# Kernel tuning notes

Measured on AMD Instinct MI355X. Metric: run time of the kernel, lower is better.

## Reference

```python
import jax, jax.numpy as jnp
import numpy as np

H, D = 8, 16
HD = H * D
SCALE0 = float(1.0 / np.sqrt(D * 1))   # degree-0 dot-product scale (order m=1)
SCALE1 = float(1.0 / np.sqrt(D * 3))   # degree-1 dot-product scale (order m=3)
SHARED = float(np.sqrt(0.5))           # shared_scale = sqrt(1/2) for DOT_PROD + SHARED
NEG = -1e9


def _split_heads_q(x):  # (b,n,HD,m) -> (b,H,n,D,m)
    b, n, _, m = x.shape
    return x.reshape(b, n, H, D, m).transpose(0, 2, 1, 3, 4)


def _split_heads_k(x):  # (b,n,N,HD,m) -> (b,H,n,N,D,m)
    b, n, N, _, m = x.shape
    return x.reshape(b, n, N, H, D, m).transpose(0, 3, 1, 2, 4, 5)


def _augment_kv(k, v, feats, W_self, null_k, null_v):
    # attend_self: VNLinear self key/value; use_null_kv: learned null tokens.
    b, n = feats.shape[:2]
    m = feats.shape[-1]
    skv = jnp.einsum('oc,bncm->bnom', W_self, feats)          # (b,n,2HD,m)
    sk, sv = jnp.split(skv, 2, axis=-2)
    sk = _split_heads_q(sk)[:, :, :, None]                     # (b,H,n,1,D,m)
    sv = _split_heads_q(sv)[:, :, :, None]
    nk = jnp.broadcast_to(null_k[None, :, None, None], (b, H, n, 1, D, m))
    nv = jnp.broadcast_to(null_v[None, :, None, None], (b, H, n, 1, D, m))
    k = jnp.concatenate([nk, sk, k], axis=3)                   # (b,H,n,2+N,D,m)
    v = jnp.concatenate([nv, sv, v], axis=3)
    return k, v


def _merge_heads(x):  # (b,H,n,D,m) -> (b,n,HD,m)
    b, _, n, _, m = x.shape
    return x.transpose(0, 2, 1, 3, 4).reshape(b, n, HD, m)


def _forward(q0, k0, v0, q1, k1, v1, feats0, feats1, edges,
             W_self_kv0, W_self_kv1, W_bias, self_bias, null_bias,
             null_k0, null_v0, null_k1, null_v1, head_weights1,
             W_out0, W_out1, neighbor_mask):
    b, n, N = edges.shape[:3]
    q0h, k0h, v0h = _split_heads_q(q0), _split_heads_k(k0), _split_heads_k(v0)
    q1h, k1h, v1h = _split_heads_q(q1), _split_heads_k(k1), _split_heads_k(v1)
    k0h, v0h = _augment_kv(k0h, v0h, feats0, W_self_kv0, null_k0, null_v0)
    k1h, v1h = _augment_kv(k1h, v1h, feats1, W_self_kv1, null_k1, null_v1)

    # pair bias for degree 0 (to_order==1); prepend null/self bias columns
    edge_bias = jnp.einsum('bnje,he->bhnj', edges, W_bias)     # (b,H,n,N)
    nb = jnp.broadcast_to(null_bias[None, :, None, None], (b, H, n, 1))
    sb = jnp.broadcast_to(self_bias[None, :, None, None], (b, H, n, 1))
    bias = jnp.concatenate([nb, sb, edge_bias], axis=-1)        # (b,H,n,2+N)

    sim0 = jnp.einsum('bhndm,bhnjdm->bhnj', q0h, k0h) * SCALE0 + bias
    w1 = jax.nn.softplus(head_weights1)                         # (1,H,1,1)
    sim1 = jnp.einsum('bhndm,bhnjdm->bhnj', q1h, k1h) * (SCALE1 * w1)

    total = (sim0 + sim1) * SHARED
    mask = jnp.concatenate(
        [jnp.ones((b, 1, n, 2), dtype=bool),                    # null + self always valid
         neighbor_mask[:, None]], axis=-1)
    total = jnp.where(mask, total, NEG)
    attn = jax.nn.softmax(total, axis=-1)                       # shared across degrees

    out0 = _merge_heads(jnp.einsum('bhnj,bhnjdm->bhndm', attn, v0h))
    out1 = _merge_heads(jnp.einsum('bhnj,bhnjdm->bhndm', attn, v1h))

    y0 = jnp.einsum('oc,bncm->bnom', W_out0, out0)              # FiberLinear deg 0
    y1 = jnp.einsum('oc,bncm->bnom', W_out1, out1)              # FiberLinear deg 1
    return y0, y1


def setup_inputs() -> dict:
    key = jax.random.key(0)
    ks = jax.random.split(key, 20)
    b, n, N, e = 1, 2048, 32, 32
    d0, d1 = 128, 64
    f = lambda k, s: jax.random.normal(k, s, dtype=jnp.float32) * 0.1
    return {
        'q0': f(ks[0], (b, n, HD, 1)), 'k0': f(ks[1], (b, n, N, HD, 1)), 'v0': f(ks[2], (b, n, N, HD, 1)),
        'q1': f(ks[3], (b, n, HD, 3)), 'k1': f(ks[4], (b, n, N, HD, 3)), 'v1': f(ks[5], (b, n, N, HD, 3)),
        'feats0': f(ks[6], (b, n, d0, 1)), 'feats1': f(ks[7], (b, n, d1, 3)),
        'edges': f(ks[8], (b, n, N, e)),
        'W_self_kv0': f(ks[9], (2 * HD, d0)), 'W_self_kv1': f(ks[10], (2 * HD, d1)),
        'W_bias': f(ks[11], (H, e)),
        'self_bias': jnp.zeros((H,), jnp.float32), 'null_bias': jnp.zeros((H,), jnp.float32),
        'null_k0': jnp.zeros((H, D, 1), jnp.float32), 'null_v0': jnp.zeros((H, D, 1), jnp.float32),
        'null_k1': jnp.zeros((H, D, 3), jnp.float32), 'null_v1': jnp.zeros((H, D, 3), jnp.float32),
        'head_weights1': jnp.full((1, H, 1, 1), float(np.log(np.e - 1.0)), jnp.float32),
        'W_out0': f(ks[12], (d0, HD)), 'W_out1': f(ks[13], (d1, HD)),
        'neighbor_mask': jax.random.uniform(ks[14], (b, n, N)) > 0.1,
    }


def reference(q0, k0, v0, q1, k1, v1, feats0, feats1, edges,
              W_self_kv0, W_self_kv1, W_bias, self_bias, null_bias,
              null_k0, null_v0, null_k1, null_v1, head_weights1,
              W_out0, W_out1, neighbor_mask):
    return _forward(q0, k0, v0, q1, k1, v1, feats0, feats1, edges,
                    W_self_kv0, W_self_kv1, W_bias, self_bias, null_bias,
                    null_k0, null_v0, null_k1, null_v1, head_weights1,
                    W_out0, W_out1, neighbor_mask)
```

## Files before the change

kernel.cpp:

```cpp
#include <hip/hip_runtime.h>

constexpr int kH  = 8;
constexpr int kD  = 16;
constexpr int kHD = 128;
constexpr int kN  = 32;
constexpr int kE  = 32;
constexpr int kD0 = 128;
constexpr int kD1 = 64;

constexpr float SCALE0   = 0.25f;
constexpr float SCALE1   = 0.14433756729740643f;
constexpr float SHARED_S = 0.70710678118654752f;
constexpr float NEGV     = -1e9f;

__global__ __launch_bounds__(256, 4) void se3_fused(
    const float* __restrict__ q0, const float* __restrict__ q1,
    const float* __restrict__ k0, const float* __restrict__ k1,
    const float* __restrict__ v0, const float* __restrict__ v1,
    const float* __restrict__ feats0, const float* __restrict__ feats1,
    const float* __restrict__ edges,
    const float* __restrict__ Wskv0, const float* __restrict__ Wskv1,
    const float* __restrict__ Wbias,
    const float* __restrict__ sbias, const float* __restrict__ nbias,
    const float* __restrict__ nk0, const float* __restrict__ nk1,
    const float* __restrict__ nv0, const float* __restrict__ nv1,
    const float* __restrict__ hw1,
    const float* __restrict__ Wout0, const float* __restrict__ Wout1,
    const int* __restrict__ nmask,
    float* __restrict__ out, int n_total)
{
  const int i = blockIdx.x;
  const int t = threadIdx.x;
  const int q4 = t & 3;
  const int qg = t >> 2;
  const int hB = qg & 7;
  const int jl = qg >> 3;

  __shared__ __align__(16) float f0s[kD0];
  __shared__ __align__(16) float f1s[kD1 * 3];
  __shared__ __align__(16) float q0s[kHD];
  __shared__ __align__(16) float q1s[kHD * 3];
  __shared__ float edg[kN * (kE + 1)];
  __shared__ float wbs[kH * kE];
  __shared__ float w1s[kH];
  __shared__ int   nmL[kN];
  __shared__ float sk0[kHD];
  __shared__ __align__(16) float sk1[kHD * 3];
  __shared__ __align__(16) float sv0[kHD];
  __shared__ __align__(16) float sv1[kHD * 3];
  __shared__ float sc[kH][36];
  __shared__ __align__(16) float o0p[2][kHD];
  __shared__ __align__(16) float o1p[2][kHD * 3];

  float4 fqv = {0.f, 0.f, 0.f, 0.f};
  if (t < 32)        fqv = ((const float4*)(feats0 + (size_t)i * kD0))[t];
  else if (t < 80)   fqv = ((const float4*)(feats1 + (size_t)i * kD1 * 3))[t - 32];
  else if (t < 112)  fqv = ((const float4*)(q0 + (size_t)i * kHD))[t - 80];
  else if (t < 208)  fqv = ((const float4*)(q1 + (size_t)i * kHD * 3))[t - 112];
  float4 ev = ((const float4*)(edges + (size_t)i * kN * kE))[t];
  float wv  = Wbias[t];
  int   nmv = (t < kN) ? nmask[(size_t)i * kN + t] : 0;
  float hv  = (t < kH) ? hw1[t] : 0.f;

  const float* k0base = k0 + (size_t)i * kN * kHD + hB * kD + q4 * 4;
  const float* k1base = k1 + (size_t)i * kN * kHD * 3 + hB * 48 + q4 * 4;
  float4 kv0[4];
  float4 kv1[4][3];
  #pragma unroll
  for (int pp = 0; pp < 4; ++pp) {
    const int j = pp * 8 + jl;
    kv0[pp] = *((const float4*)(k0base + (size_t)j * kHD));
    #pragma unroll
    for (int pc = 0; pc < 3; ++pc)
      kv1[pp][pc] = *((const float4*)(k1base + (size_t)j * kHD * 3 + pc * 16));
  }
  __builtin_amdgcn_sched_barrier(0);

  if (t < 32)        ((float4*)f0s)[t] = fqv;
  else if (t < 80)   ((float4*)f1s)[t - 32] = fqv;
  else if (t < 112)  ((float4*)q0s)[t - 80] = fqv;
  else if (t < 208)  ((float4*)q1s)[t - 112] = fqv;
  { int j = t >> 3, e4 = (t & 7) * 4;
    float* dst = &edg[j * 33 + e4];
    dst[0] = ev.x; dst[1] = ev.y; dst[2] = ev.z; dst[3] = ev.w; }
  wbs[t] = wv;
  if (t < kN) nmL[t] = nmv;
  if (t < kH) w1s[t] = log1pf(expf(hv));
  __syncthreads();

  #pragma unroll
  for (int pass = 0; pass < 4; ++pass) {
    const int r = qg + 64 * pass;
    const float4* w0r = (const float4*)(Wskv0 + (size_t)r * kD0);
    float a0 = 0.f;
    #pragma unroll
    for (int g = 0; g < 8; ++g) {
      float4 w = w0r[q4 + 4 * g]; int c = (q4 + 4 * g) * 4;
      a0 += w.x * f0s[c] + w.y * f0s[c + 1]
          + w.z * f0s[c + 2] + w.w * f0s[c + 3];
    }
    const float4* w1r = (const float4*)(Wskv1 + (size_t)r * kD1);
    float a1[3] = {};
    #pragma unroll
    for (int g = 0; g < 4; ++g) {
      float4 w = w1r[q4 + 4 * g]; int c = (q4 + 4 * g) * 4;
      float wvv[4] = {w.x, w.y, w.z, w.w};
      #pragma unroll
      for (int k = 0; k < 4; ++k) {
        const float* fp = &f1s[(c + k) * 3];
        a1[0] += wvv[k] * fp[0];
        a1[1] += wvv[k] * fp[1];
        a1[2] += wvv[k] * fp[2];
      }
    }
    a0 += __shfl_xor(a0, 1); a0 += __shfl_xor(a0, 2);
    #pragma unroll
    for (int c = 0; c < 3; ++c) {
      a1[c] += __shfl_xor(a1[c], 1);
      a1[c] += __shfl_xor(a1[c], 2);
    }
    if (q4 == 0) {
      if (r < kHD) {
        sk0[r] = a0;
        sk1[r * 3 + 0] = a1[0]; sk1[r * 3 + 1] = a1[1]; sk1[r * 3 + 2] = a1[2];
      } else {
        const int o = r - kHD;
        sv0[o] = a0;
        sv1[o * 3 + 0] = a1[0]; sv1[o * 3 + 1] = a1[1]; sv1[o * 3 + 2] = a1[2];
      }
    }
  }
  __syncthreads();

  if (t < 16) {
    const int h = t & 7;
    const bool is_self = t >= 8;
    float s0 = 0.f, s1 = 0.f, bias;
    if (is_self) {
      #pragma unroll
      for (int d = 0; d < kD; ++d) s0 += q0s[h * kD + d] * sk0[h * kD + d];
      #pragma unroll
      for (int x = 0; x < 48; ++x) s1 += q1s[h * 48 + x] * sk1[h * 48 + x];
      bias = sbias[h];
    } else {
      #pragma unroll
      for (int d = 0; d < kD; ++d) s0 += q0s[h * kD + d] * nk0[h * kD + d];
      #pragma unroll
      for (int x = 0; x < 48; ++x) s1 += q1s[h * 48 + x] * nk1[h * 48 + x];
      bias = nbias[h];
    }
    sc[h][is_self ? 1 : 0] =
        (s0 * SCALE0 + bias + s1 * SCALE1 * w1s[h]) * SHARED_S;
  }

  {
    const float w1h = w1s[hB];
    float wbf[8];
    #pragma unroll
    for (int e = 0; e < 8; ++e) wbf[e] = wbs[hB * kE + q4 * 8 + e];
    const float4 q0f = *((const float4*)(q0s + hB * kD) + q4);
    float4 q1f[3];
    #pragma unroll
    for (int pc = 0; pc < 3; ++pc)
      q1f[pc] = *((const float4*)(q1s + hB * 48 + pc * 16) + q4);

    #pragma unroll
    for (int pp = 0; pp < 4; ++pp) {
      const int j = pp * 8 + jl;
      float s0 = kv0[pp].x * q0f.x + kv0[pp].y * q0f.y
               + kv0[pp].z * q0f.z + kv0[pp].w * q0f.w;
      float s1 = 0.f;
      #pragma unroll
      for (int pc = 0; pc < 3; ++pc)
        s1 += kv1[pp][pc].x * q1f[pc].x + kv1[pp][pc].y * q1f[pc].y
            + kv1[pp][pc].z * q1f[pc].z + kv1[pp][pc].w * q1f[pc].w;
      float bias = 0.f;
      #pragma unroll
      for (int e = 0; e < 8; ++e) bias += edg[j * 33 + q4 * 8 + e] * wbf[e];

      float part = s0 * SCALE0 + bias + s1 * SCALE1 * w1h;
      part += __shfl_xor(part, 1);
      part += __shfl_xor(part, 2);
      if (q4 == 0) sc[hB][2 + j] = nmL[j] ? part * SHARED_S : NEGV;
    }
  }
  __syncthreads();

  if (t < 128) {
    const int h = t >> 4, l = t & 15;
    float* rp = sc[h];
    float va = rp[2 + l], vb = rp[2 + l + 16];
    float mx = fmaxf(va, vb);
    #pragma unroll
    for (int off = 8; off > 0; off >>= 1) mx = fmaxf(mx, __shfl_xor(mx, off));
    float e0v = rp[0], e1v = rp[1];
    mx = fmaxf(mx, fmaxf(e0v, e1v));
    float ea = __expf(va - mx), eb = __expf(vb - mx);
    float sum = ea + eb;
    #pragma unroll
    for (int off = 8; off > 0; off >>= 1) sum += __shfl_xor(sum, off);
    float ee0 = __expf(e0v - mx), ee1 = __expf(e1v - mx);
    float inv = 1.f / (sum + ee0 + ee1);
    rp[2 + l] = ea * inv;
    rp[2 + l + 16] = eb * inv;
    if (l == 0) rp[0] = ee0 * inv;
    if (l == 1) rp[1] = ee1 * inv;
  }
  __syncthreads();

  {
    const int halfD = t >> 7;
    const int s = t & 127;
    float4 acc = {0.f, 0.f, 0.f, 0.f};
    if (s < 32) {
      const int h = s >> 2;
      const float* at = sc[h];
      if (halfD == 0) {
        float4 nv = ((const float4*)nv0)[s];
        float4 sv = ((const float4*)sv0)[s];
        acc.x = at[0] * nv.x + at[1] * sv.x;
        acc.y = at[0] * nv.y + at[1] * sv.y;
        acc.z = at[0] * nv.z + at[1] * sv.z;
        acc.w = at[0] * nv.w + at[1] * sv.w;
      }
      const float4* vp = (const float4*)(v0 + (size_t)i * kN * kHD) + s;
      float4 vbuf[8];
      #pragma unroll
      for (int gg = 0; gg < 2; ++gg) {
        const int g = halfD * 2 + gg;
        #pragma unroll
        for (int r = 0; r < 8; ++r) vbuf[r] = vp[(g * 8 + r) * 32];
        #pragma unroll
        for (int r = 0; r < 8; ++r) {
          float a = at[2 + g * 8 + r];
          acc.x += a * vbuf[r].x; acc.y += a * vbuf[r].y;
          acc.z += a * vbuf[r].z; acc.w += a * vbuf[r].w;
        }
      }
      ((float4*)o0p[halfD])[s] = acc;
    } else {
      const int s1 = s - 32;
      const int h = s1 / 12;
      const float* at = sc[h];
      if (halfD == 0) {
        float4 nv = ((const float4*)nv1)[s1];
        float4 sv = ((const float4*)sv1)[s1];
        acc.x = at[0] * nv.x + at[1] * sv.x;
        acc.y = at[0] * nv.y + at[1] * sv.y;
        acc.z = at[0] * nv.z + at[1] * sv.z;
        acc.w = at[0] * nv.w + at[1] * sv.w;
      }
      const float4* vp = (const float4*)(v1 + (size_t)i * kN * kHD * 3) + s1;
      float4 vbuf[8];
      #pragma unroll
      for (int gg = 0; gg < 2; ++gg) {
        const int g = halfD * 2 + gg;
        #pragma unroll
        for (int r = 0; r < 8; ++r) vbuf[r] = vp[(g * 8 + r) * 96];
        #pragma unroll
        for (int r = 0; r < 8; ++r) {
          float a = at[2 + g * 8 + r];
          acc.x += a * vbuf[r].x; acc.y += a * vbuf[r].y;
          acc.z += a * vbuf[r].z; acc.w += a * vbuf[r].w;
        }
      }
      ((float4*)o1p[halfD])[s1] = acc;
    }
  }
  __syncthreads();

  if (t < 128) {
    if (t < 32) {
      float4 a = ((float4*)o0p[0])[t], b = ((float4*)o0p[1])[t];
      a.x += b.x; a.y += b.y; a.z += b.z; a.w += b.w;
      ((float4*)o0p[0])[t] = a;
    } else {
      const int s1 = t - 32;
      float4 a = ((float4*)o1p[0])[s1], b = ((float4*)o1p[1])[s1];
      a.x += b.x; a.y += b.y; a.z += b.z; a.w += b.w;
      ((float4*)o1p[0])[s1] = a;
    }
  }
  __syncthreads();

  #pragma unroll
  for (int pass = 0; pass < 5; ++pass) {
    const int u = qg + 64 * pass;
    if (u < 128) {
      const float4* wr = (const float4*)(Wout0 + (size_t)u * kHD);
      float a = 0.f;
      #pragma unroll
      for (int g = 0; g < 8; ++g) {
        float4 w = wr[q4 + 4 * g]; int c = (q4 + 4 * g) * 4;
        a += w.x * o0p[0][c] + w.y * o0p[0][c + 1]
           + w.z * o0p[0][c + 2] + w.w * o0p[0][c + 3];
      }
      a += __shfl_xor(a, 1); a += __shfl_xor(a, 2);
      if (q4 == 0) out[(size_t)i * kHD + u] = a;
    } else {
      const int v2 = u - 128, o = v2 / 3, m = v2 - o * 3;
      const float4* wr = (const float4*)(Wout1 + (size_t)o * kHD);
      float a = 0.f;
      #pragma unroll
      for (int g = 0; g < 8; ++g) {
        float4 w = wr[q4 + 4 * g]; int c = (q4 + 4 * g) * 4;
        a += w.x * o1p[0][(c + 0) * 3 + m] + w.y * o1p[0][(c + 1) * 3 + m]
           + w.z * o1p[0][(c + 2) * 3 + m] + w.w * o1p[0][(c + 3) * 3 + m];
      }
      a += __shfl_xor(a, 1); a += __shfl_xor(a, 2);
      if (q4 == 0)
        out[(size_t)n_total * kHD + (size_t)i * 192 + v2] = a;
    }
  }
}

extern "C" void kernel_launch(void* const* d_in, const int* in_sizes, int n_in,
                              void* d_out, int out_size, void* d_ws, size_t ws_size,
                              hipStream_t stream) {
  const int n = in_sizes[0] / kHD;
  const float* q0     = (const float*)d_in[0];
  const float* k0     = (const float*)d_in[1];
  const float* v0     = (const float*)d_in[2];
  const float* q1     = (const float*)d_in[3];
  const float* k1     = (const float*)d_in[4];
  const float* v1     = (const float*)d_in[5];
  const float* feats0 = (const float*)d_in[6];
  const float* feats1 = (const float*)d_in[7];
  const float* edges  = (const float*)d_in[8];
  const float* Wskv0  = (const float*)d_in[9];
  const float* Wskv1  = (const float*)d_in[10];
  const float* Wbias  = (const float*)d_in[11];
  const float* sbias  = (const float*)d_in[12];
  const float* nbias  = (const float*)d_in[13];
  const float* nk0    = (const float*)d_in[14];
  const float* nv0    = (const float*)d_in[15];
  const float* nk1    = (const float*)d_in[16];
  const float* nv1    = (const float*)d_in[17];
  const float* hw1    = (const float*)d_in[18];
  const float* Wout0  = (const float*)d_in[19];
  const float* Wout1  = (const float*)d_in[20];
  const int*   nmask  = (const int*)d_in[21];

  se3_fused<<<n, 256, 0, stream>>>(
      q0, q1, k0, k1, v0, v1, feats0, feats1, edges,
      Wskv0, Wskv1, Wbias, sbias, nbias, nk0, nk1, nv0, nv1, hw1,
      Wout0, Wout1, nmask, (float*)d_out, n);
}
```

Measured before the change: 356.6 us.

## Defer K loads to the score phase and raise occupancy target to 8 blocks

The early prefetch of the K tiles (16 float4 per thread) is moved from the kernel prologue to just before the score computation, and the sched_barrier is removed. This frees registers across the self-KV projection phase, and launch_bounds is raised to 8 blocks per CU to trade register budget for occupancy. The cost is that K load latency is no longer overlapped with the prologue and projection work, so it must be hidden by other resident waves instead.

```diff
diff --git a/kernel.cpp b/kernel.cpp
--- a/kernel.cpp
+++ b/kernel.cpp
@@ -13,7 +13,7 @@
 constexpr float SHARED_S = 0.70710678118654752f;
 constexpr float NEGV     = -1e9f;
 
-__global__ __launch_bounds__(256, 4) void se3_fused(
+__global__ __launch_bounds__(256, 8) void se3_fused(
     const float* __restrict__ q0, const float* __restrict__ q1,
     const float* __restrict__ k0, const float* __restrict__ k1,
     const float* __restrict__ v0, const float* __restrict__ v1,
@@ -52,40 +52,22 @@
   __shared__ __align__(16) float o0p[2][kHD];
   __shared__ __align__(16) float o1p[2][kHD * 3];
 
-  float4 fqv = {0.f, 0.f, 0.f, 0.f};
-  if (t < 32)        fqv = ((const float4*)(feats0 + (size_t)i * kD0))[t];
-  else if (t < 80)   fqv = ((const float4*)(feats1 + (size_t)i * kD1 * 3))[t - 32];
-  else if (t < 112)  fqv = ((const float4*)(q0 + (size_t)i * kHD))[t - 80];
-  else if (t < 208)  fqv = ((const float4*)(q1 + (size_t)i * kHD * 3))[t - 112];
-  float4 ev = ((const float4*)(edges + (size_t)i * kN * kE))[t];
-  float wv  = Wbias[t];
-  int   nmv = (t < kN) ? nmask[(size_t)i * kN + t] : 0;
-  float hv  = (t < kH) ? hw1[t] : 0.f;
-
-  const float* k0base = k0 + (size_t)i * kN * kHD + hB * kD + q4 * 4;
-  const float* k1base = k1 + (size_t)i * kN * kHD * 3 + hB * 48 + q4 * 4;
-  float4 kv0[4];
-  float4 kv1[4][3];
-  #pragma unroll
-  for (int pp = 0; pp < 4; ++pp) {
-    const int j = pp * 8 + jl;
-    kv0[pp] = *((const float4*)(k0base + (size_t)j * kHD));
-    #pragma unroll
-    for (int pc = 0; pc < 3; ++pc)
-      kv1[pp][pc] = *((const float4*)(k1base + (size_t)j * kHD * 3 + pc * 16));
-  }
-  __builtin_amdgcn_sched_barrier(0);
-
-  if (t < 32)        ((float4*)f0s)[t] = fqv;
-  else if (t < 80)   ((float4*)f1s)[t - 32] = fqv;
-  else if (t < 112)  ((float4*)q0s)[t - 80] = fqv;
-  else if (t < 208)  ((float4*)q1s)[t - 112] = fqv;
-  { int j = t >> 3, e4 = (t & 7) * 4;
+  if (t < 32) {
+    ((float4*)f0s)[t] = ((const float4*)(feats0 + (size_t)i * kD0))[t];
+  } else if (t < 80) {
+    ((float4*)f1s)[t - 32] = ((const float4*)(feats1 + (size_t)i * kD1 * 3))[t - 32];
+  } else if (t < 112) {
+    ((float4*)q0s)[t - 80] = ((const float4*)(q0 + (size_t)i * kHD))[t - 80];
+  } else if (t < 208) {
+    ((float4*)q1s)[t - 112] = ((const float4*)(q1 + (size_t)i * kHD * 3))[t - 112];
+  }
+  { float4 ev = ((const float4*)(edges + (size_t)i * kN * kE))[t];
+    int j = t >> 3, e4 = (t & 7) * 4;
     float* dst = &edg[j * 33 + e4];
     dst[0] = ev.x; dst[1] = ev.y; dst[2] = ev.z; dst[3] = ev.w; }
-  wbs[t] = wv;
-  if (t < kN) nmL[t] = nmv;
-  if (t < kH) w1s[t] = log1pf(expf(hv));
+  wbs[t] = Wbias[t];
+  if (t < kN) nmL[t] = nmask[(size_t)i * kN + t];
+  if (t < kH) w1s[t] = log1pf(expf(hw1[t]));
   __syncthreads();
 
   #pragma unroll
@@ -163,6 +145,20 @@
     #pragma unroll
     for (int pc = 0; pc < 3; ++pc)
       q1f[pc] = *((const float4*)(q1s + hB * 48 + pc * 16) + q4);
+
+    const float* k0base = k0 + (size_t)i * kN * kHD + hB * kD + q4 * 4;
+    const float* k1base = k1 + (size_t)i * kN * kHD * 3 + hB * 48 + q4 * 4;
+
+    float4 kv0[4];
+    float4 kv1[4][3];
+    #pragma unroll
+    for (int pp = 0; pp < 4; ++pp) {
+      const int j = pp * 8 + jl;
+      kv0[pp] = *((const float4*)(k0base + (size_t)j * kHD));
+      #pragma unroll
+      for (int pc = 0; pc < 3; ++pc)
+        kv1[pp][pc] = *((const float4*)(k1base + (size_t)j * kHD * 3 + pc * 16));
+    }
 
     #pragma unroll
     for (int pp = 0; pp < 4; ++pp) {
```

New measurement: 382.8 us. +7.3%, slower.
